# Optimization experiments

Measured on AMD Instinct MI355X. Metric: run time of the kernel, lower is better.

Reference implementation:

```python
import jax, jax.numpy as jnp
import numpy as np

B, L, D, U = 4, 1024, 64, 32

def setup_inputs() -> dict:
    key = jax.random.key(0)
    ks = jax.random.split(key, 6)
    inputs = jax.random.normal(ks[0], (B, L, D), dtype=jnp.float32)
    Wt = jax.random.normal(ks[1], (D, U), dtype=jnp.float32) * 0.1
    Wx = jax.random.normal(ks[2], (D, U), dtype=jnp.float32) * 0.1
    Wa = jax.random.normal(ks[3], (U, 1), dtype=jnp.float32) * 0.1
    bh = jax.random.normal(ks[4], (U,), dtype=jnp.float32) * 0.1
    ba = jax.random.normal(ks[5], (1,), dtype=jnp.float32) * 0.1
    return {"inputs": inputs, "Wt": Wt, "Wx": Wx, "Wa": Wa,
            "bh": bh, "ba": ba, "attention_width": 0}

def reference(inputs, Wt, Wx, Wa, bh, ba, attention_width):
    # Additive (Bahdanau) self-attention emission.
    q = inputs @ Wt                              # (B, L, U)
    k = inputs @ Wx                              # (B, L, U)
    # broadcast add -> (B, L, L, U), the dominant intermediate
    h = jnp.tanh(q[:, :, None, :] + k[:, None, :, :] + bh)
    e = jnp.squeeze(h @ Wa, axis=-1) + ba        # (B, L, L); ba broadcasts
    # NOTE: attention_width mask is dead code in the original forward -> ignored.
    # manual max-subtracted softmax with +1e-8 denominator (as in source)
    m = jnp.max(e, axis=-1, keepdims=True)
    ex = jnp.exp(e - m)
    a = ex / (jnp.sum(ex, axis=-1, keepdims=True) + 1e-8)
    v = jnp.einsum('bij,bjd->bid', a, inputs)    # (B, L, D)
    return v
```

## Files before the change

kernel.cpp:

```cpp
#include <hip/hip_runtime.h>

#define BB 4
#define LL 1024
#define DD 64
#define UU 32
#define TI 4

__global__ __launch_bounds__(256) void precompute_kernel(
    const float* __restrict__ inp, const float* __restrict__ Wt,
    const float* __restrict__ Wx, const float* __restrict__ bh,
    float* __restrict__ Eq, float* __restrict__ Ek)
{
    __shared__ float s_in[8][DD];
    __shared__ float s_wt[DD][UU];
    __shared__ float s_wx[DD][UU];
    int t = threadIdx.x;
    int row0 = blockIdx.x * 8;
    if (t < 128)
        ((float4*)s_in)[t] = ((const float4*)(inp + (size_t)row0 * DD))[t];
#pragma unroll
    for (int p = 0; p < 2; ++p) {
        ((float4*)s_wt)[p * 256 + t] = ((const float4*)Wt)[p * 256 + t];
        ((float4*)s_wx)[p * 256 + t] = ((const float4*)Wx)[p * 256 + t];
    }
    __syncthreads();
    int r = t >> 5;
    int u = t & 31;
    size_t row = row0 + r;
    float q = 0.f, k = 0.f;
#pragma unroll
    for (int d = 0; d < DD; ++d) {
        float x = s_in[r][d];
        q = fmaf(x, s_wt[d][u], q);
        k = fmaf(x, s_wx[d][u], k);
    }
    Eq[row * UU + u] = __expf(2.f * (q + bh[u]));
    Ek[row * UU + u] = __expf(2.f * k);
}

union ShMem {
    float  a[LL][TI];
    float4 v[16][TI][16];
};

__global__ __launch_bounds__(256) void attn_kernel(
    const float* __restrict__ Eq, const float* __restrict__ Ek,
    const float* __restrict__ inp, const float* __restrict__ Wa,
    float* __restrict__ out)
{
    __shared__ ShMem sh;
    __shared__ float s_red[8][TI];

    int t  = threadIdx.x;
    int w  = t >> 6;
    int b  = blockIdx.x >> 8;
    int i0 = (blockIdx.x & 255) * TI;

    const float4* ekb4 = (const float4*)(Ek + (size_t)b * LL * UU);
    const float*  eqb  = Eq + ((size_t)(b * LL + i0)) * UU;

    float acc[TI][4];
#pragma unroll
    for (int i = 0; i < TI; ++i)
#pragma unroll
        for (int jj = 0; jj < 4; ++jj) acc[i][jj] = 0.f;

    const float4* ekp[4];
#pragma unroll
    for (int jj = 0; jj < 4; ++jj) ekp[jj] = ekb4 + (size_t)(jj * 256 + t) * 8;

    float4 cur[4], nxt[4];
#pragma unroll
    for (int jj = 0; jj < 4; ++jj) cur[jj] = ekp[jj][0];

#pragma unroll
    for (int u4 = 0; u4 < 8; ++u4) {
        if (u4 < 7) {
#pragma unroll
            for (int jj = 0; jj < 4; ++jj) nxt[jj] = ekp[jj][u4 + 1];
        }
#pragma unroll
        for (int i = 0; i < TI; ++i) {
            const float* eqq = eqb + i * UU + u4 * 4;
            float eq0 = eqq[0], eq1 = eqq[1], eq2 = eqq[2], eq3 = eqq[3];
            const float* waq = Wa + u4 * 4;
            float wa0 = waq[0], wa1 = waq[1], wa2 = waq[2], wa3 = waq[3];
#pragma unroll
            for (int jj = 0; jj < 4; ++jj) {
                float4 ek = cur[jj];
                float p  = fmaf(eq0, ek.x, 1.f);
                float q  = fmaf(eq1, ek.y, 1.f);
                float r  = fmaf(eq2, ek.z, 1.f);
                float s  = fmaf(eq3, ek.w, 1.f);
                float n01 = fmaf(wa0, q, wa1 * p);
                float n23 = fmaf(wa2, s, wa3 * r);
                float pq = p * q, rs = r * s;
                float num = fmaf(n01, rs, n23 * pq);
                float den = pq * rs;
                acc[i][jj] = fmaf(num, __builtin_amdgcn_rcpf(den), acc[i][jj]);
            }
        }
        if (u4 < 7) {
#pragma unroll
            for (int jj = 0; jj < 4; ++jj) cur[jj] = nxt[jj];
        }
    }

    float ev[TI][4];
#pragma unroll
    for (int i = 0; i < TI; ++i)
#pragma unroll
        for (int jj = 0; jj < 4; ++jj) ev[i][jj] = -2.f * acc[i][jj];

    float wred[TI];
#pragma unroll
    for (int i = 0; i < TI; ++i) {
        float v = fmaxf(fmaxf(ev[i][0], ev[i][1]), fmaxf(ev[i][2], ev[i][3]));
#pragma unroll
        for (int m = 32; m >= 1; m >>= 1) v = fmaxf(v, __shfl_xor(v, m, 64));
        wred[i] = v;
    }
    if ((t & 63) == 0) {
#pragma unroll
        for (int i = 0; i < TI; ++i) s_red[w][i] = wred[i];
    }
    __syncthreads();
    float m[TI];
#pragma unroll
    for (int i = 0; i < TI; ++i)
        m[i] = fmaxf(fmaxf(s_red[0][i], s_red[1][i]),
                     fmaxf(s_red[2][i], s_red[3][i]));

#pragma unroll
    for (int i = 0; i < TI; ++i) {
        float s = 0.f;
#pragma unroll
        for (int jj = 0; jj < 4; ++jj) {
            ev[i][jj] = __expf(ev[i][jj] - m[i]);
            s += ev[i][jj];
        }
#pragma unroll
        for (int mm = 32; mm >= 1; mm >>= 1) s += __shfl_xor(s, mm, 64);
        wred[i] = s;
    }
    if ((t & 63) == 0) {
#pragma unroll
        for (int i = 0; i < TI; ++i) s_red[4 + w][i] = wred[i];
    }
    __syncthreads();
    float rs[TI];
#pragma unroll
    for (int i = 0; i < TI; ++i) {
        float s = ((s_red[4][i] + s_red[5][i]) + (s_red[6][i] + s_red[7][i]));
        rs[i] = 1.0f / (s + 1e-8f);
    }

#pragma unroll
    for (int jj = 0; jj < 4; ++jj) {
        float4 av;
        av.x = ev[0][jj] * rs[0];
        av.y = ev[1][jj] * rs[1];
        av.z = ev[2][jj] * rs[2];
        av.w = ev[3][jj] * rs[3];
        ((float4*)sh.a)[jj * 256 + t] = av;
    }
    __syncthreads();

    int dq = t & 15;
    int g  = t >> 4;
    const float4* inp4 = (const float4*)(inp + (size_t)b * LL * DD);
    float4 v0 = {0,0,0,0}, v1 = {0,0,0,0}, v2 = {0,0,0,0}, v3 = {0,0,0,0};
#pragma unroll 4
    for (int jj = 0; jj < 64; ++jj) {
        int j = jj * 16 + g;
        float4 x  = inp4[j * 16 + dq];
        float4 av = ((const float4*)sh.a)[j];
        v0.x = fmaf(av.x, x.x, v0.x); v0.y = fmaf(av.x, x.y, v0.y);
        v0.z = fmaf(av.x, x.z, v0.z); v0.w = fmaf(av.x, x.w, v0.w);
        v1.x = fmaf(av.y, x.x, v1.x); v1.y = fmaf(av.y, x.y, v1.y);
        v1.z = fmaf(av.y, x.z, v1.z); v1.w = fmaf(av.y, x.w, v1.w);
        v2.x = fmaf(av.z, x.x, v2.x); v2.y = fmaf(av.z, x.y, v2.y);
        v2.z = fmaf(av.z, x.z, v2.z); v2.w = fmaf(av.z, x.w, v2.w);
        v3.x = fmaf(av.w, x.x, v3.x); v3.y = fmaf(av.w, x.y, v3.y);
        v3.z = fmaf(av.w, x.z, v3.z); v3.w = fmaf(av.w, x.w, v3.w);
    }
    __syncthreads();
    sh.v[g][0][dq] = v0;
    sh.v[g][1][dq] = v1;
    sh.v[g][2][dq] = v2;
    sh.v[g][3][dq] = v3;
    __syncthreads();

    int i = t >> 6;
    int d = t & 63;
    const float* svf = (const float*)sh.v;
    float r = 0.f;
#pragma unroll
    for (int g2 = 0; g2 < 16; ++g2) r += svf[g2 * 256 + i * 64 + d];
    out[((size_t)b * LL + (i0 + i)) * DD + d] = r;
}

extern "C" void kernel_launch(void* const* d_in, const int* in_sizes, int n_in,
                              void* d_out, int out_size, void* d_ws, size_t ws_size,
                              hipStream_t stream) {
    const float* inp = (const float*)d_in[0];
    const float* Wt  = (const float*)d_in[1];
    const float* Wx  = (const float*)d_in[2];
    const float* Wa  = (const float*)d_in[3];
    const float* bh  = (const float*)d_in[4];
    float* out = (float*)d_out;

    float* Eq = (float*)d_ws;
    float* Ek = Eq + (size_t)BB * LL * UU;

    precompute_kernel<<<BB * LL / 8, 256, 0, stream>>>(inp, Wt, Wx, bh, Eq, Ek);
    attn_kernel<<<BB * LL / TI, 256, 0, stream>>>(Eq, Ek, inp, Wa, out);
}
```

Before: 100.8 us.

## Process eight query rows per block with 512 threads and shuffle-reduce PV partials

Raises the query rows per attention block from four to eight and the block size to 512 threads. Each thread now covers two key columns instead of four, and the Wa loads are hoisted out of the inner row loop. The P·V stage accumulates eight output rows per thread and does a wave-level shuffle reduction before the shared-memory cross-wave sum. The aim is better reuse of each Ek and input load across more query rows and a lighter final reduction. In exchange the grid is halved to 512 blocks and each thread holds more registers, which may lower occupancy.

```diff
diff --git a/kernel.cpp b/kernel.cpp
--- a/kernel.cpp
+++ b/kernel.cpp
@@ -4,7 +4,8 @@
 #define LL 1024
 #define DD 64
 #define UU 32
-#define TI 4
+#define TI 8
+#define NT 512
 
 __global__ __launch_bounds__(256) void precompute_kernel(
     const float* __restrict__ inp, const float* __restrict__ Wt,
@@ -39,55 +40,47 @@
 }
 
 union ShMem {
-    float  a[LL][TI];
-    float4 v[16][TI][16];
+    struct { float a0[LL][4]; float a1[LL][4]; } a;
+    float4 v[8][TI][16];
 };
 
-__global__ __launch_bounds__(256) void attn_kernel(
+__global__ __launch_bounds__(NT) void attn_kernel(
     const float* __restrict__ Eq, const float* __restrict__ Ek,
     const float* __restrict__ inp, const float* __restrict__ Wa,
     float* __restrict__ out)
 {
     __shared__ ShMem sh;
-    __shared__ float s_red[8][TI];
+    __shared__ float s_red[2][8][TI];
 
     int t  = threadIdx.x;
     int w  = t >> 6;
-    int b  = blockIdx.x >> 8;
-    int i0 = (blockIdx.x & 255) * TI;
+    int b  = blockIdx.x >> 7;
+    int i0 = (blockIdx.x & 127) * TI;
 
     const float4* ekb4 = (const float4*)(Ek + (size_t)b * LL * UU);
     const float*  eqb  = Eq + ((size_t)(b * LL + i0)) * UU;
 
-    float acc[TI][4];
-#pragma unroll
-    for (int i = 0; i < TI; ++i)
-#pragma unroll
-        for (int jj = 0; jj < 4; ++jj) acc[i][jj] = 0.f;
-
-    const float4* ekp[4];
-#pragma unroll
-    for (int jj = 0; jj < 4; ++jj) ekp[jj] = ekb4 + (size_t)(jj * 256 + t) * 8;
-
-    float4 cur[4], nxt[4];
-#pragma unroll
-    for (int jj = 0; jj < 4; ++jj) cur[jj] = ekp[jj][0];
+    float acc[TI][2];
+#pragma unroll
+    for (int i = 0; i < TI; ++i) { acc[i][0] = 0.f; acc[i][1] = 0.f; }
+
+    const float4* ekp0 = ekb4 + (size_t)t * 8;
+    const float4* ekp1 = ekb4 + (size_t)(NT + t) * 8;
+    float4 cur0 = ekp0[0], cur1 = ekp1[0];
 
 #pragma unroll
     for (int u4 = 0; u4 < 8; ++u4) {
-        if (u4 < 7) {
-#pragma unroll
-            for (int jj = 0; jj < 4; ++jj) nxt[jj] = ekp[jj][u4 + 1];
-        }
+        float4 nxt0, nxt1;
+        if (u4 < 7) { nxt0 = ekp0[u4 + 1]; nxt1 = ekp1[u4 + 1]; }
+        const float* waq = Wa + u4 * 4;
+        float wa0 = waq[0], wa1 = waq[1], wa2 = waq[2], wa3 = waq[3];
 #pragma unroll
         for (int i = 0; i < TI; ++i) {
             const float* eqq = eqb + i * UU + u4 * 4;
             float eq0 = eqq[0], eq1 = eqq[1], eq2 = eqq[2], eq3 = eqq[3];
-            const float* waq = Wa + u4 * 4;
-            float wa0 = waq[0], wa1 = waq[1], wa2 = waq[2], wa3 = waq[3];
-#pragma unroll
-            for (int jj = 0; jj < 4; ++jj) {
-                float4 ek = cur[jj];
+#pragma unroll
+            for (int jj = 0; jj < 2; ++jj) {
+                float4 ek = jj ? cur1 : cur0;
                 float p  = fmaf(eq0, ek.x, 1.f);
                 float q  = fmaf(eq1, ek.y, 1.f);
                 float r  = fmaf(eq2, ek.z, 1.f);
@@ -100,95 +93,117 @@
                 acc[i][jj] = fmaf(num, __builtin_amdgcn_rcpf(den), acc[i][jj]);
             }
         }
-        if (u4 < 7) {
-#pragma unroll
-            for (int jj = 0; jj < 4; ++jj) cur[jj] = nxt[jj];
-        }
-    }
-
-    float ev[TI][4];
-#pragma unroll
-    for (int i = 0; i < TI; ++i)
-#pragma unroll
-        for (int jj = 0; jj < 4; ++jj) ev[i][jj] = -2.f * acc[i][jj];
+        if (u4 < 7) { cur0 = nxt0; cur1 = nxt1; }
+    }
+
+    float ev[TI][2];
+#pragma unroll
+    for (int i = 0; i < TI; ++i) {
+        ev[i][0] = -2.f * acc[i][0];
+        ev[i][1] = -2.f * acc[i][1];
+    }
 
     float wred[TI];
 #pragma unroll
     for (int i = 0; i < TI; ++i) {
-        float v = fmaxf(fmaxf(ev[i][0], ev[i][1]), fmaxf(ev[i][2], ev[i][3]));
+        float v = fmaxf(ev[i][0], ev[i][1]);
 #pragma unroll
         for (int m = 32; m >= 1; m >>= 1) v = fmaxf(v, __shfl_xor(v, m, 64));
         wred[i] = v;
     }
     if ((t & 63) == 0) {
 #pragma unroll
-        for (int i = 0; i < TI; ++i) s_red[w][i] = wred[i];
+        for (int i = 0; i < TI; ++i) s_red[0][w][i] = wred[i];
     }
     __syncthreads();
     float m[TI];
 #pragma unroll
-    for (int i = 0; i < TI; ++i)
-        m[i] = fmaxf(fmaxf(s_red[0][i], s_red[1][i]),
-                     fmaxf(s_red[2][i], s_red[3][i]));
-
-#pragma unroll
-    for (int i = 0; i < TI; ++i) {
-        float s = 0.f;
-#pragma unroll
-        for (int jj = 0; jj < 4; ++jj) {
-            ev[i][jj] = __expf(ev[i][jj] - m[i]);
-            s += ev[i][jj];
-        }
+    for (int i = 0; i < TI; ++i) {
+        float v = s_red[0][0][i];
+#pragma unroll
+        for (int w2 = 1; w2 < 8; ++w2) v = fmaxf(v, s_red[0][w2][i]);
+        m[i] = v;
+    }
+
+#pragma unroll
+    for (int i = 0; i < TI; ++i) {
+        ev[i][0] = __expf(ev[i][0] - m[i]);
+        ev[i][1] = __expf(ev[i][1] - m[i]);
+        float s = ev[i][0] + ev[i][1];
 #pragma unroll
         for (int mm = 32; mm >= 1; mm >>= 1) s += __shfl_xor(s, mm, 64);
         wred[i] = s;
     }
     if ((t & 63) == 0) {
 #pragma unroll
-        for (int i = 0; i < TI; ++i) s_red[4 + w][i] = wred[i];
+        for (int i = 0; i < TI; ++i) s_red[1][w][i] = wred[i];
     }
     __syncthreads();
     float rs[TI];
 #pragma unroll
     for (int i = 0; i < TI; ++i) {
-        float s = ((s_red[4][i] + s_red[5][i]) + (s_red[6][i] + s_red[7][i]));
+        float s = 0.f;
+#pragma unroll
+        for (int w2 = 0; w2 < 8; ++w2) s += s_red[1][w2][i];
         rs[i] = 1.0f / (s + 1e-8f);
     }
 
 #pragma unroll
-    for (int jj = 0; jj < 4; ++jj) {
-        float4 av;
-        av.x = ev[0][jj] * rs[0];
-        av.y = ev[1][jj] * rs[1];
-        av.z = ev[2][jj] * rs[2];
-        av.w = ev[3][jj] * rs[3];
-        ((float4*)sh.a)[jj * 256 + t] = av;
+    for (int jj = 0; jj < 2; ++jj) {
+        int j = jj * NT + t;
+        float4 lo, hi;
+        lo.x = ev[0][jj] * rs[0]; lo.y = ev[1][jj] * rs[1];
+        lo.z = ev[2][jj] * rs[2]; lo.w = ev[3][jj] * rs[3];
+        hi.x = ev[4][jj] * rs[4]; hi.y = ev[5][jj] * rs[5];
+        hi.z = ev[6][jj] * rs[6]; hi.w = ev[7][jj] * rs[7];
+        *(float4*)(&sh.a.a0[j][0]) = lo;
+        *(float4*)(&sh.a.a1[j][0]) = hi;
     }
     __syncthreads();
 
     int dq = t & 15;
     int g  = t >> 4;
     const float4* inp4 = (const float4*)(inp + (size_t)b * LL * DD);
-    float4 v0 = {0,0,0,0}, v1 = {0,0,0,0}, v2 = {0,0,0,0}, v3 = {0,0,0,0};
+    float4 v[TI];
+#pragma unroll
+    for (int i = 0; i < TI; ++i) v[i] = (float4){0.f, 0.f, 0.f, 0.f};
+
 #pragma unroll 4
-    for (int jj = 0; jj < 64; ++jj) {
-        int j = jj * 16 + g;
+    for (int jj = 0; jj < 32; ++jj) {
+        int j = jj * 32 + g;
         float4 x  = inp4[j * 16 + dq];
-        float4 av = ((const float4*)sh.a)[j];
-        v0.x = fmaf(av.x, x.x, v0.x); v0.y = fmaf(av.x, x.y, v0.y);
-        v0.z = fmaf(av.x, x.z, v0.z); v0.w = fmaf(av.x, x.w, v0.w);
-        v1.x = fmaf(av.y, x.x, v1.x); v1.y = fmaf(av.y, x.y, v1.y);
-        v1.z = fmaf(av.y, x.z, v1.z); v1.w = fmaf(av.y, x.w, v1.w);
-        v2.x = fmaf(av.z, x.x, v2.x); v2.y = fmaf(av.z, x.y, v2.y);
-        v2.z = fmaf(av.z, x.z, v2.z); v2.w = fmaf(av.z, x.w, v2.w);
-        v3.x = fmaf(av.w, x.x, v3.x); v3.y = fmaf(av.w, x.y, v3.y);
-        v3.z = fmaf(av.w, x.z, v3.z); v3.w = fmaf(av.w, x.w, v3.w);
-    }
-    __syncthreads();
-    sh.v[g][0][dq] = v0;
-    sh.v[g][1][dq] = v1;
-    sh.v[g][2][dq] = v2;
-    sh.v[g][3][dq] = v3;
+        float4 a0 = *(const float4*)(&sh.a.a0[j][0]);
+        float4 a1 = *(const float4*)(&sh.a.a1[j][0]);
+        v[0].x = fmaf(a0.x, x.x, v[0].x); v[0].y = fmaf(a0.x, x.y, v[0].y);
+        v[0].z = fmaf(a0.x, x.z, v[0].z); v[0].w = fmaf(a0.x, x.w, v[0].w);
+        v[1].x = fmaf(a0.y, x.x, v[1].x); v[1].y = fmaf(a0.y, x.y, v[1].y);
+        v[1].z = fmaf(a0.y, x.z, v[1].z); v[1].w = fmaf(a0.y, x.w, v[1].w);
+        v[2].x = fmaf(a0.z, x.x, v[2].x); v[2].y = fmaf(a0.z, x.y, v[2].y);
+        v[2].z = fmaf(a0.z, x.z, v[2].z); v[2].w = fmaf(a0.z, x.w, v[2].w);
+        v[3].x = fmaf(a0.w, x.x, v[3].x); v[3].y = fmaf(a0.w, x.y, v[3].y);
+        v[3].z = fmaf(a0.w, x.z, v[3].z); v[3].w = fmaf(a0.w, x.w, v[3].w);
+        v[4].x = fmaf(a1.x, x.x, v[4].x); v[4].y = fmaf(a1.x, x.y, v[4].y);
+        v[4].z = fmaf(a1.x, x.z, v[4].z); v[4].w = fmaf(a1.x, x.w, v[4].w);
+        v[5].x = fmaf(a1.y, x.x, v[5].x); v[5].y = fmaf(a1.y, x.y, v[5].y);
+        v[5].z = fmaf(a1.y, x.z, v[5].z); v[5].w = fmaf(a1.y, x.w, v[5].w);
+        v[6].x = fmaf(a1.z, x.x, v[6].x); v[6].y = fmaf(a1.z, x.y, v[6].y);
+        v[6].z = fmaf(a1.z, x.z, v[6].z); v[6].w = fmaf(a1.z, x.w, v[6].w);
+        v[7].x = fmaf(a1.w, x.x, v[7].x); v[7].y = fmaf(a1.w, x.y, v[7].y);
+        v[7].z = fmaf(a1.w, x.z, v[7].z); v[7].w = fmaf(a1.w, x.w, v[7].w);
+    }
+
+#pragma unroll
+    for (int i = 0; i < TI; ++i) {
+        v[i].x += __shfl_xor(v[i].x, 16, 64); v[i].y += __shfl_xor(v[i].y, 16, 64);
+        v[i].z += __shfl_xor(v[i].z, 16, 64); v[i].w += __shfl_xor(v[i].w, 16, 64);
+        v[i].x += __shfl_xor(v[i].x, 32, 64); v[i].y += __shfl_xor(v[i].y, 32, 64);
+        v[i].z += __shfl_xor(v[i].z, 32, 64); v[i].w += __shfl_xor(v[i].w, 32, 64);
+    }
+    __syncthreads();
+    if ((t & 63) < 16) {
+#pragma unroll
+        for (int i = 0; i < TI; ++i) sh.v[w][i][dq] = v[i];
+    }
     __syncthreads();
 
     int i = t >> 6;
@@ -196,7 +211,7 @@
     const float* svf = (const float*)sh.v;
     float r = 0.f;
 #pragma unroll
-    for (int g2 = 0; g2 < 16; ++g2) r += svf[g2 * 256 + i * 64 + d];
+    for (int w2 = 0; w2 < 8; ++w2) r += svf[w2 * (TI * 64) + i * 64 + d];
     out[((size_t)b * LL + (i0 + i)) * DD + d] = r;
 }
 
@@ -214,5 +229,5 @@
     float* Ek = Eq + (size_t)BB * LL * UU;
 
     precompute_kernel<<<BB * LL / 8, 256, 0, stream>>>(inp, Wt, Wx, bh, Eq, Ek);
-    attn_kernel<<<BB * LL / TI, 256, 0, stream>>>(Eq, Ek, inp, Wa, out);
+    attn_kernel<<<BB * LL / TI, NT, 0, stream>>>(Eq, Ek, inp, Wa, out);
 }
```

New measurement: 98.43 us. -2.4%, faster.
